# Optimization experiments

Hardware: AMD Instinct MI355X
Metric: run time of the kernel (lower is better)

## Reference

```python
import jax, jax.numpy as jnp
import numpy as np

CAPACITY_FACTOR = 1.0

def setup_inputs() -> dict:
    key = jax.random.key(0)
    ks = jax.random.split(key, 5)
    B, S, D, E, F = 2, 2048, 1024, 8, 4096
    x = jax.random.normal(ks[0], (B, S, D), dtype=jnp.float32)
    Ws = jax.random.normal(ks[1], (D, E), dtype=jnp.float32) * (1.0 / np.sqrt(D))
    bs = jnp.zeros((E,), dtype=jnp.float32)
    W1 = jax.random.normal(ks[2], (E, D, F), dtype=jnp.float32) * (1.0 / np.sqrt(D))
    b1 = jnp.zeros((E, F), dtype=jnp.float32)
    W2 = jax.random.normal(ks[3], (E, F, D), dtype=jnp.float32) * (1.0 / np.sqrt(F))
    b2 = jnp.zeros((E, D), dtype=jnp.float32)
    return {"x": x, "Ws": Ws, "bs": bs, "W1": W1, "b1": b1, "W2": W2, "b2": b2}

def reference(x, Ws, bs, W1, b1, W2, b2):
    B, S, D = x.shape
    E = Ws.shape[1]
    N = B * S
    k = int(CAPACITY_FACTOR * N / E)  # expert-choice capacity
    xf = x.reshape(N, D)
    # switch gating: [N, E] -> [E, N]
    route_prob = jax.nn.softmax(xf @ Ws + bs, axis=-1).T
    # expert-choice top-k tokens per expert: values/indices [E, k]
    route_vals, routes = jax.lax.top_k(route_prob, k)
    # dispatch: gather per-expert token blocks [E, k, D]
    xin = xf[routes]
    # per-expert FFN (grouped GEMM): Linear -> GELU -> Linear
    h = jax.nn.gelu(jnp.einsum('ekd,edf->ekf', xin, W1) + b1[:, None, :])
    out = jnp.einsum('ekf,efd->ekd', h, W2) + b2[:, None, :]
    # scale by routing prob (is_scale_prob=True)
    out = out * route_vals[..., None]
    # combine: scatter-add into token buffer (== sum over the E-indexed zero tensor)
    final = jnp.zeros((N, D), dtype=x.dtype).at[routes.reshape(-1)].add(out.reshape(-1, D))
    return final.reshape(B, S, D)
```

## Files before the change

### kernel.cpp

```cpp
#include <hip/hip_runtime.h>
#include <hip/hip_bf16.h>

#define N_TOK 4096
#define DIM   1024
#define NEXP  8
#define FDIM  4096
#define KCAP  512

typedef __attribute__((ext_vector_type(8))) short bf16x8;
typedef __attribute__((ext_vector_type(4))) float floatx4;

__device__ inline unsigned short f2bf(float f) {
  union { float f; unsigned int i; } v; v.f = f;
  unsigned int r = v.i + 0x7fffu + ((v.i >> 16) & 1u);
  return (unsigned short)(r >> 16);
}

__device__ inline void ld2lds16(const void* g, void* l) {
  __builtin_amdgcn_global_load_lds(
      (const __attribute__((address_space(1))) unsigned int*)g,
      (__attribute__((address_space(3))) unsigned int*)l,
      16, 0, 0);
}

__global__ __launch_bounds__(256)
void prep_kernel(const float* __restrict__ x,
                 const float* __restrict__ Ws,
                 const float* __restrict__ bs,
                 float* __restrict__ probs_t,
                 unsigned short* __restrict__ xb,
                 const float* __restrict__ W1, unsigned short* __restrict__ w1t,
                 const float* __restrict__ W2, unsigned short* __restrict__ w2t) {
  __shared__ unsigned short tile[32][40];
  int bid = blockIdx.x;
  int t = threadIdx.x;

  if (bid >= 1024) {
    const float* src; unsigned short* dst; int R, C, bx, by, bz;
    int b = bid - 1024;
    if (b < 32768) {
      src = W1; dst = w1t; R = DIM; C = FDIM;
      bx = b & 127; by = (b >> 7) & 31; bz = b >> 12;
    } else {
      b -= 32768;
      src = W2; dst = w2t; R = FDIM; C = DIM;
      bx = b & 31; by = (b >> 5) & 127; bz = b >> 12;
    }
    size_t off = (size_t)bz * R * C;
    int r0 = by * 32, c0 = bx * 32;
    int tr = t >> 3, tc = (t & 7) * 4;
    float4 v = *(const float4*)&src[off + (size_t)(r0 + tr) * C + (c0 + tc)];
    tile[tr][tc + 0] = f2bf(v.x);
    tile[tr][tc + 1] = f2bf(v.y);
    tile[tr][tc + 2] = f2bf(v.z);
    tile[tr][tc + 3] = f2bf(v.w);
    __syncthreads();
    ushort4 o;
    o.x = tile[tc + 0][tr];
    o.y = tile[tc + 1][tr];
    o.z = tile[tc + 2][tr];
    o.w = tile[tc + 3][tr];
    *(ushort4*)&dst[off + (size_t)(c0 + tr) * R + (r0 + tc)] = o;
    return;
  }

  int token = bid * 4 + (t >> 6);
  int lane  = t & 63;
  const float* xr = x + (size_t)token * DIM;
  unsigned short* xbr = xb + (size_t)token * DIM;
  double acc[NEXP];
#pragma unroll
  for (int e = 0; e < NEXP; e++) acc[e] = 0.0;
#pragma unroll
  for (int c = 0; c < 4; c++) {
    int d0 = (c * 64 + lane) * 4;
    float4 xv = *(const float4*)&xr[d0];
    ushort4 ob;
    ob.x = f2bf(xv.x); ob.y = f2bf(xv.y); ob.z = f2bf(xv.z); ob.w = f2bf(xv.w);
    *(ushort4*)&xbr[d0] = ob;
    float xa[4] = {xv.x, xv.y, xv.z, xv.w};
#pragma unroll
    for (int q = 0; q < 4; q++) {
      const float* wr = &Ws[(size_t)(d0 + q) * NEXP];
      float4 w0 = *(const float4*)&wr[0];
      float4 w1 = *(const float4*)&wr[4];
      double xs = (double)xa[q];
      acc[0] += xs * (double)w0.x; acc[1] += xs * (double)w0.y;
      acc[2] += xs * (double)w0.z; acc[3] += xs * (double)w0.w;
      acc[4] += xs * (double)w1.x; acc[5] += xs * (double)w1.y;
      acc[6] += xs * (double)w1.z; acc[7] += xs * (double)w1.w;
    }
  }
#pragma unroll
  for (int off = 32; off > 0; off >>= 1)
#pragma unroll
    for (int e = 0; e < NEXP; e++) acc[e] += __shfl_down(acc[e], off, 64);
  if (lane == 0) {
    double mx = -1e300;
#pragma unroll
    for (int e = 0; e < NEXP; e++) { acc[e] += (double)bs[e]; if (acc[e] > mx) mx = acc[e]; }
    double s = 0.0, p[NEXP];
#pragma unroll
    for (int e = 0; e < NEXP; e++) { p[e] = exp(acc[e] - mx); s += p[e]; }
#pragma unroll
    for (int e = 0; e < NEXP; e++) probs_t[(size_t)e * N_TOK + token] = (float)(p[e] / s);
  }
}

__global__ __launch_bounds__(1024)
void topk_kernel(const float* __restrict__ probs_t, int* __restrict__ routes,
                 float* __restrict__ vals, int* __restrict__ counts,
                 int* __restrict__ inv) {
  int e = blockIdx.x;
  const float* P = probs_t + (size_t)e * N_TOK;
  __shared__ int hist[4096];
  __shared__ int hist2[4096];
  __shared__ int scan[1024];
  __shared__ int sB, sR, sCnt;
  __shared__ unsigned int sPrefix, sMask;
  int t = threadIdx.x;

  float vv[4];
  unsigned int vb[4];
  float4 v4 = *(const float4*)&P[t * 4];
  vv[0] = v4.x; vv[1] = v4.y; vv[2] = v4.z; vv[3] = v4.w;
#pragma unroll
  for (int q = 0; q < 4; q++) vb[q] = __float_as_uint(vv[q]);

  if (t == 0) { sR = KCAP; sPrefix = 0u; sMask = 0u; sCnt = 0; }
  __syncthreads();

  for (int level = 0; level < 3; level++) {
    int nb    = (level < 2) ? 4096 : 256;
    int shift = (level == 0) ? 20 : (level == 1) ? 8 : 0;
    for (int i = t; i < nb; i += 1024) hist[i] = 0;
    __syncthreads();
    unsigned int msk = sMask, pfx = sPrefix;
#pragma unroll
    for (int q = 0; q < 4; q++)
      if ((vb[q] & msk) == pfx)
        atomicAdd(&hist[(vb[q] >> shift) & (nb - 1)], 1);
    __syncthreads();
    int* src = hist; int* dst = hist2;
    for (int d = 1; d < nb; d <<= 1) {
      for (int i = t; i < nb; i += 1024)
        dst[i] = src[i] + ((i + d < nb) ? src[i + d] : 0);
      int* tmp = src; src = dst; dst = tmp;
      __syncthreads();
    }
    int R = sR;
    for (int i = t; i < nb; i += 1024) {
      int si = src[i];
      int sn = (i + 1 < nb) ? src[i + 1] : 0;
      if (si >= R && sn < R) sB = i;
    }
    __syncthreads();
    if (t == 0) {
      int B = sB;
      int strict = (B + 1 < nb) ? src[B + 1] : 0;
      sR = sR - strict;
      sPrefix |= ((unsigned int)B) << shift;
      sMask   |= ((unsigned int)(nb - 1)) << shift;
    }
    __syncthreads();
  }

  unsigned int T = sPrefix;
  int R = sR;
  int cnt = 0;
#pragma unroll
  for (int q = 0; q < 4; q++) if (vb[q] == T) cnt++;
  scan[t] = cnt;
  __syncthreads();
  for (int d = 1; d < 1024; d <<= 1) {
    int v = (t >= d) ? scan[t - d] : 0;
    __syncthreads();
    scan[t] += v;
    __syncthreads();
  }
  int grank = scan[t] - cnt;
#pragma unroll
  for (int q = 0; q < 4; q++) {
    bool sel = false;
    if (vb[q] > T) sel = true;
    else if (vb[q] == T) { if (grank < R) sel = true; grank++; }
    if (sel) {
      int pos = atomicAdd(&sCnt, 1);
      int slot = e * KCAP + pos;
      int token = t * 4 + q;
      routes[slot] = token;
      vals[slot]   = vv[q];
      int pc = atomicAdd(&counts[token], 1);
      inv[token * NEXP + pc] = slot;
    }
  }
}

__global__ __launch_bounds__(256, 3)
void gemm1_kernel(const unsigned short* __restrict__ xb,
                  const unsigned short* __restrict__ w1t,
                  const float* __restrict__ b1,
                  const int* __restrict__ routes,
                  unsigned short* __restrict__ h) {
  int lb = blockIdx.x;
  int sb = ((lb & 7) << 7) | (lb >> 3);
  int nt = sb & 31, mt = (sb >> 5) & 3, e = sb >> 7;
  __shared__ unsigned short smem[16384];
  unsigned short* As = smem;
  unsigned short* Bs = smem + 8192;
  int t = threadIdx.x, lane = t & 63, wave = t >> 6;
  int wm = (wave >> 1) * 64, wn = (wave & 1) * 64;
  int fr = lane & 15, fq = lane >> 4;
  int lrow = lane >> 3, lchunk = (lane & 7) ^ (lrow & 7);
  int sw = fr & 7;

  const unsigned short* aP[4];
  const unsigned short* bP[4];
#pragma unroll
  for (int q = 0; q < 4; q++) {
    int m = wave * 4 + q;
    int row = m * 8 + lrow;
    int token = routes[e * KCAP + mt * 128 + row];
    aP[q] = xb + (size_t)token * DIM + lchunk * 8;
    bP[q] = w1t + ((size_t)e * FDIM + nt * 128 + row) * DIM + lchunk * 8;
  }

  floatx4 acc[4][4];
#pragma unroll
  for (int i = 0; i < 4; i++)
#pragma unroll
    for (int j = 0; j < 4; j++) acc[i][j] = (floatx4)0.0f;

  for (int k0 = 0; k0 < DIM; k0 += 64) {
    __syncthreads();
#pragma unroll
    for (int q = 0; q < 4; q++) {
      int m = wave * 4 + q;
      ld2lds16(aP[q] + k0, As + m * 512);
      ld2lds16(bP[q] + k0, Bs + m * 512);
    }
    __syncthreads();
#pragma unroll
    for (int ks = 0; ks < 2; ks++) {
      bf16x8 af[4], bf[4];
      int cs = ((ks << 2) | fq) ^ sw;
#pragma unroll
      for (int i = 0; i < 4; i++)
        af[i] = *(const bf16x8*)&As[(wm + i * 16 + fr) * 64 + cs * 8];
#pragma unroll
      for (int j = 0; j < 4; j++)
        bf[j] = *(const bf16x8*)&Bs[(wn + j * 16 + fr) * 64 + cs * 8];
#pragma unroll
      for (int i = 0; i < 4; i++)
#pragma unroll
        for (int j = 0; j < 4; j++)
          acc[i][j] = __builtin_amdgcn_mfma_f32_16x16x32_bf16(af[i], bf[j], acc[i][j], 0, 0, 0);
    }
  }

  float bias[4];
#pragma unroll
  for (int j = 0; j < 4; j++) bias[j] = b1[e * FDIM + nt * 128 + wn + j * 16 + fr];
  float* LC = (float*)smem;
#pragma unroll
  for (int p = 0; p < 2; p++) {
    __syncthreads();
    if ((wn >> 6) == p) {
#pragma unroll
      for (int i = 0; i < 4; i++)
#pragma unroll
        for (int r = 0; r < 4; r++) {
          int lr = wm + i * 16 + fq * 4 + r;
#pragma unroll
          for (int j = 0; j < 4; j++) {
            float v = acc[i][j][r] + bias[j];
            float u = 0.7978845608028654f * (v + 0.044715f * v * v * v);
            LC[lr * 64 + j * 16 + fr] = v * __builtin_amdgcn_rcpf(1.0f + __expf(-2.0f * u));
          }
        }
    }
    __syncthreads();
    int row = t >> 1, ch = (t & 1) * 32;
    size_t hb = (((size_t)e * 64 + nt * 2 + p) * KCAP + mt * 128 + row) * 64 + ch;
    const float* lrow2 = &LC[row * 64 + ch];
#pragma unroll
    for (int qq = 0; qq < 4; qq++) {
      bf16x8 o;
#pragma unroll
      for (int u8 = 0; u8 < 8; u8++) o[u8] = (short)f2bf(lrow2[qq * 8 + u8]);
      *(bf16x8*)&h[hb + qq * 8] = o;
    }
  }
}

__global__ __launch_bounds__(256, 3)
void gemm2_kernel(const unsigned short* __restrict__ h,
                  const unsigned short* __restrict__ w2t,
                  const float* __restrict__ b2,
                  const float* __restrict__ vals,
                  float* __restrict__ partials) {
  int lb = blockIdx.x;
  int sb = ((lb & 7) << 6) | (lb >> 3);
  int nt = sb & 7, mt = (sb >> 3) & 3, z = sb >> 5;
  int e = z >> 1, s = z & 1;
  __shared__ unsigned short smem[16384];
  unsigned short* As = smem;
  unsigned short* Bs = smem + 8192;
  int t = threadIdx.x, lane = t & 63, wave = t >> 6;
  int wm = (wave >> 1) * 64, wn = (wave & 1) * 64;
  int fr = lane & 15, fq = lane >> 4;
  int lrow = lane >> 3, lchunk = (lane & 7) ^ (lrow & 7);
  int sw = fr & 7;

  const unsigned short* aP[4];
  const unsigned short* bP[4];
#pragma unroll
  for (int q = 0; q < 4; q++) {
    int m = wave * 4 + q;
    int row = m * 8 + lrow;
    aP[q] = h + (((size_t)e * 64 + s * 32) * KCAP + mt * 128 + row) * 64 + lchunk * 8;
    bP[q] = w2t + ((size_t)e * DIM + nt * 128 + row) * FDIM + s * 2048 + lchunk * 8;
  }

  floatx4 acc[4][4];
#pragma unroll
  for (int i = 0; i < 4; i++)
#pragma unroll
    for (int j = 0; j < 4; j++) acc[i][j] = (floatx4)0.0f;

  for (int k0 = 0; k0 < 2048; k0 += 64) {
    __syncthreads();
#pragma unroll
    for (int q = 0; q < 4; q++) {
      int m = wave * 4 + q;
      ld2lds16(aP[q] + (size_t)k0 * 512, As + m * 512);
      ld2lds16(bP[q] + k0, Bs + m * 512);
    }
    __syncthreads();
#pragma unroll
    for (int ks = 0; ks < 2; ks++) {
      bf16x8 af[4], bf[4];
      int cs = ((ks << 2) | fq) ^ sw;
#pragma unroll
      for (int i = 0; i < 4; i++)
        af[i] = *(const bf16x8*)&As[(wm + i * 16 + fr) * 64 + cs * 8];
#pragma unroll
      for (int j = 0; j < 4; j++)
        bf[j] = *(const bf16x8*)&Bs[(wn + j * 16 + fr) * 64 + cs * 8];
#pragma unroll
      for (int i = 0; i < 4; i++)
#pragma unroll
        for (int j = 0; j < 4; j++)
          acc[i][j] = __builtin_amdgcn_mfma_f32_16x16x32_bf16(af[i], bf[j], acc[i][j], 0, 0, 0);
    }
  }

  float* LC = (float*)smem;
  float* outp = partials + (size_t)s * N_TOK * DIM;
  int slotbase = e * KCAP + mt * 128;
  float bias[4];
#pragma unroll
  for (int j = 0; j < 4; j++)
    bias[j] = (s == 0) ? b2[e * DIM + nt * 128 + wn + j * 16 + fr] : 0.0f;
#pragma unroll
  for (int p = 0; p < 2; p++) {
    __syncthreads();
    if ((wn >> 6) == p) {
#pragma unroll
      for (int i = 0; i < 4; i++)
#pragma unroll
        for (int r = 0; r < 4; r++) {
          int lr = wm + i * 16 + fq * 4 + r;
          float vs = vals[slotbase + lr];
#pragma unroll
          for (int j = 0; j < 4; j++)
            LC[lr * 64 + j * 16 + fr] = (acc[i][j][r] + bias[j]) * vs;
        }
    }
    __syncthreads();
    int row = t >> 1, ch = (t & 1) * 32;
    float* dst = outp + (size_t)(slotbase + row) * DIM + nt * 128 + p * 64 + ch;
#pragma unroll
    for (int qq = 0; qq < 8; qq++)
      *(float4*)&dst[qq * 4] = *(const float4*)&LC[row * 64 + ch + qq * 4];
  }
}

__global__ __launch_bounds__(256)
void combine_kernel(const float* __restrict__ partials, const int* __restrict__ counts,
                    const int* __restrict__ inv, float* __restrict__ out) {
  int token = blockIdx.x;
  int t = threadIdx.x;
  int c = counts[token];
  float4 acc = {0.f, 0.f, 0.f, 0.f};
  for (int i = 0; i < c; i++) {
    int slot = inv[token * NEXP + i];
    const float* base = partials + (size_t)slot * DIM + t * 4;
#pragma unroll
    for (int s = 0; s < 2; s++) {
      float4 v = *(const float4*)&base[(size_t)s * N_TOK * DIM];
      acc.x += v.x; acc.y += v.y; acc.z += v.z; acc.w += v.w;
    }
  }
  *(float4*)&out[(size_t)token * DIM + t * 4] = acc;
}

extern "C" void kernel_launch(void* const* d_in, const int* in_sizes, int n_in,
                              void* d_out, int out_size, void* d_ws, size_t ws_size,
                              hipStream_t stream) {
  const float* x  = (const float*)d_in[0];
  const float* Ws = (const float*)d_in[1];
  const float* bs = (const float*)d_in[2];
  const float* W1 = (const float*)d_in[3];
  const float* b1 = (const float*)d_in[4];
  const float* W2 = (const float*)d_in[5];
  const float* b2 = (const float*)d_in[6];
  float* out = (float*)d_out;

  char* ws = (char*)d_ws;
  unsigned short* w1t = (unsigned short*)ws; ws += (size_t)NEXP * FDIM * DIM * 2;
  unsigned short* w2t = (unsigned short*)ws; ws += (size_t)NEXP * DIM * FDIM * 2;
  unsigned short* h   = (unsigned short*)ws; ws += (size_t)NEXP * KCAP * FDIM * 2;
  char* pshare = ws; ws += (size_t)2 * N_TOK * DIM * 4;
  unsigned short* xb = (unsigned short*)pshare;
  float* partials    = (float*)pshare;
  float* probs  = (float*)ws; ws += (size_t)NEXP * N_TOK * 4;
  int*   routes = (int*)ws;   ws += NEXP * KCAP * 4;
  float* vals   = (float*)ws; ws += NEXP * KCAP * 4;
  int*   counts = (int*)ws;   ws += N_TOK * 4;
  int*   inv    = (int*)ws;   ws += N_TOK * NEXP * 4;

  hipMemsetAsync(counts, 0, N_TOK * sizeof(int), stream);
  prep_kernel<<<1024 + 32768 + 32768, 256, 0, stream>>>(x, Ws, bs, probs, xb,
                                                        W1, w1t, W2, w2t);
  topk_kernel<<<NEXP, 1024, 0, stream>>>(probs, routes, vals, counts, inv);
  gemm1_kernel<<<1024, 256, 0, stream>>>(xb, w1t, b1, routes, h);
  gemm2_kernel<<<512, 256, 0, stream>>>(h, w2t, b2, vals, partials);
  combine_kernel<<<N_TOK, 256, 0, stream>>>(partials, counts, inv, out);
}
```

Measured before the change: 480.5 us.

## Use 64x64 transpose tiles and share one bf16 weight buffer across both GEMMs

The weight transpose-and-convert now uses 64x64 tiles, with four float4 loads per thread and 16-byte bf16x8 stores, instead of 32x32 tiles with 8-byte stores. The goal is fewer blocks and wider, better-coalesced writes. W2's transpose moves into its own kernel that runs after gemm1 and reuses the same workspace buffer as W1's transposed copy. This halves the bf16 weight footprint and may keep more of it cache-resident. The cost is a serialized extra launch between the two GEMMs, and any overlap of the W2 conversion with the earlier stages is lost.

Measured after the change: 440.7 us. -8.3%, faster.

```diff
diff --git a/kernel.cpp b/kernel.cpp
--- a/kernel.cpp
+++ b/kernel.cpp
@@ -21,6 +21,35 @@
       (const __attribute__((address_space(1))) unsigned int*)g,
       (__attribute__((address_space(3))) unsigned int*)l,
       16, 0, 0);
+}
+
+__device__ inline void transpose64(const float* __restrict__ src,
+                                   unsigned short* __restrict__ dst,
+                                   int R, int C, int e, int by, int bx, int t,
+                                   unsigned short (*tile)[66]) {
+  size_t off = (size_t)e * R * C;
+  int r0 = by * 64, c0 = bx * 64;
+  const float* S = src + off + (size_t)r0 * C + c0;
+#pragma unroll
+  for (int p = 0; p < 4; p++) {
+    int r = (t >> 4) + p * 16, c = (t & 15) * 4;
+    float4 v = *(const float4*)&S[(size_t)r * C + c];
+    tile[r][c + 0] = f2bf(v.x);
+    tile[r][c + 1] = f2bf(v.y);
+    tile[r][c + 2] = f2bf(v.z);
+    tile[r][c + 3] = f2bf(v.w);
+  }
+  __syncthreads();
+  unsigned short* D = dst + off + (size_t)c0 * R + r0;
+#pragma unroll
+  for (int p = 0; p < 2; p++) {
+    int oc = (t >> 3) + p * 32;
+    int orr = (t & 7) * 8;
+    bf16x8 o;
+#pragma unroll
+    for (int j = 0; j < 8; j++) o[j] = (short)tile[orr + j][oc];
+    *(bf16x8*)&D[(size_t)oc * R + orr] = o;
+  }
 }
 
 __global__ __launch_bounds__(256)
@@ -29,38 +58,16 @@
                  const float* __restrict__ bs,
                  float* __restrict__ probs_t,
                  unsigned short* __restrict__ xb,
-                 const float* __restrict__ W1, unsigned short* __restrict__ w1t,
-                 const float* __restrict__ W2, unsigned short* __restrict__ w2t) {
-  __shared__ unsigned short tile[32][40];
+                 const float* __restrict__ W1, unsigned short* __restrict__ wt) {
+  __shared__ unsigned short tile[64][66];
   int bid = blockIdx.x;
   int t = threadIdx.x;
 
   if (bid >= 1024) {
-    const float* src; unsigned short* dst; int R, C, bx, by, bz;
     int b = bid - 1024;
-    if (b < 32768) {
-      src = W1; dst = w1t; R = DIM; C = FDIM;
-      bx = b & 127; by = (b >> 7) & 31; bz = b >> 12;
-    } else {
-      b -= 32768;
-      src = W2; dst = w2t; R = FDIM; C = DIM;
-      bx = b & 31; by = (b >> 5) & 127; bz = b >> 12;
-    }
-    size_t off = (size_t)bz * R * C;
-    int r0 = by * 32, c0 = bx * 32;
-    int tr = t >> 3, tc = (t & 7) * 4;
-    float4 v = *(const float4*)&src[off + (size_t)(r0 + tr) * C + (c0 + tc)];
-    tile[tr][tc + 0] = f2bf(v.x);
-    tile[tr][tc + 1] = f2bf(v.y);
-    tile[tr][tc + 2] = f2bf(v.z);
-    tile[tr][tc + 3] = f2bf(v.w);
-    __syncthreads();
-    ushort4 o;
-    o.x = tile[tc + 0][tr];
-    o.y = tile[tc + 1][tr];
-    o.z = tile[tc + 2][tr];
-    o.w = tile[tc + 3][tr];
-    *(ushort4*)&dst[off + (size_t)(c0 + tr) * R + (r0 + tc)] = o;
+    int e = b >> 10, rem = b & 1023;
+    int bx = rem & 63, by = rem >> 6;
+    transpose64(W1, wt, DIM, FDIM, e, by, bx, t, tile);
     return;
   }
 
@@ -105,6 +112,15 @@
 #pragma unroll
     for (int e = 0; e < NEXP; e++) probs_t[(size_t)e * N_TOK + token] = (float)(p[e] / s);
   }
+}
+
+__global__ __launch_bounds__(256)
+void t2_kernel(const float* __restrict__ W2, unsigned short* __restrict__ wt) {
+  __shared__ unsigned short tile[64][66];
+  int b = blockIdx.x, t = threadIdx.x;
+  int e = b >> 10, rem = b & 1023;
+  int bx = rem & 15, by = rem >> 4;
+  transpose64(W2, wt, FDIM, DIM, e, by, bx, t, tile);
 }
 
 __global__ __launch_bounds__(1024)
@@ -418,9 +434,8 @@
   float* out = (float*)d_out;
 
   char* ws = (char*)d_ws;
-  unsigned short* w1t = (unsigned short*)ws; ws += (size_t)NEXP * FDIM * DIM * 2;
-  unsigned short* w2t = (unsigned short*)ws; ws += (size_t)NEXP * DIM * FDIM * 2;
-  unsigned short* h   = (unsigned short*)ws; ws += (size_t)NEXP * KCAP * FDIM * 2;
+  unsigned short* wt = (unsigned short*)ws; ws += (size_t)NEXP * FDIM * DIM * 2;
+  unsigned short* h  = (unsigned short*)ws; ws += (size_t)NEXP * KCAP * FDIM * 2;
   char* pshare = ws; ws += (size_t)2 * N_TOK * DIM * 4;
   unsigned short* xb = (unsigned short*)pshare;
   float* partials    = (float*)pshare;
@@ -431,10 +446,10 @@
   int*   inv    = (int*)ws;   ws += N_TOK * NEXP * 4;
 
   hipMemsetAsync(counts, 0, N_TOK * sizeof(int), stream);
-  prep_kernel<<<1024 + 32768 + 32768, 256, 0, stream>>>(x, Ws, bs, probs, xb,
-                                                        W1, w1t, W2, w2t);
+  prep_kernel<<<1024 + 8192, 256, 0, stream>>>(x, Ws, bs, probs, xb, W1, wt);
   topk_kernel<<<NEXP, 1024, 0, stream>>>(probs, routes, vals, counts, inv);
-  gemm1_kernel<<<1024, 256, 0, stream>>>(xb, w1t, b1, routes, h);
-  gemm2_kernel<<<512, 256, 0, stream>>>(h, w2t, b2, vals, partials);
+  gemm1_kernel<<<1024, 256, 0, stream>>>(xb, wt, b1, routes, h);
+  t2_kernel<<<8192, 256, 0, stream>>>(W2, wt);
+  gemm2_kernel<<<512, 256, 0, stream>>>(h, wt, b2, vals, partials);
   combine_kernel<<<N_TOK, 256, 0, stream>>>(partials, counts, inv, out);
 }
```
